# Kernel tuning notes

Hardware: AMD Instinct MI355X
Metric: run time of the kernel (lower is better)

Reference implementation:

```python
import jax, jax.numpy as jnp
import numpy as np


def setup_inputs() -> dict:
    key = jax.random.key(0)
    k1, k2 = jax.random.split(key)
    B, N, M = 8, 8192, 8192
    xyz1 = jax.random.normal(k1, (B, N, 3), dtype=jnp.float32)
    xyz2 = jax.random.normal(k2, (B, M, 3), dtype=jnp.float32)
    return {"xyz1": xyz1, "xyz2": xyz2}


def reference(xyz1, xyz2):
    # (same math as the CUDA kernel's per-pair squared L2 scan).
    sq1 = jnp.sum(xyz1 * xyz1, axis=-1)              # [B, N]
    sq2 = jnp.sum(xyz2 * xyz2, axis=-1)              # [B, M]
    inner = jnp.einsum('bnd,bmd->bnm', xyz1, xyz2)   # [B, N, M]
    d = sq1[:, :, None] + sq2[:, None, :] - 2.0 * inner
    d = jnp.maximum(d, 0.0)  # guard tiny negatives from the expansion
    dist1 = jnp.min(d, axis=2)  # [B, N] nearest sq-dist in xyz2 for each xyz1 point
    dist2 = jnp.min(d, axis=1)  # [B, M] nearest sq-dist in xyz1 for each xyz2 point
    return dist1, dist2
```

## Files before the change

### kernel.cpp

```cpp
#include <hip/hip_runtime.h>
#include <math.h>


typedef __attribute__((ext_vector_type(8))) short short8;
typedef __attribute__((ext_vector_type(16))) float f32x16;

#define CTC    256
#define TILEB  (CTC * 32)
#define NGRP   (CTC / 32)
#define NSPLIT 4

__host__ __device__ static inline size_t pad512(size_t x) {
  return (x + 511) & ~(size_t)511;
}

__device__ __forceinline__ unsigned short bf16h(float x) {
  unsigned u = __float_as_uint(x);
  return (unsigned short)((u + 0x7fffu + ((u >> 16) & 1u)) >> 16);
}
__device__ __forceinline__ float bf16f(unsigned short h) {
  return __uint_as_float((unsigned)h << 16);
}
__device__ __forceinline__ float m3(float a, float b, float c) {
  return fminf(fminf(a, b), c);
}
__device__ __forceinline__ float red16(const f32x16& d, float mm) {
  float r0 = m3(d[0], d[1], d[2]);
  float r1 = m3(d[3], d[4], d[5]);
  float r2 = m3(d[6], d[7], d[8]);
  float r3 = m3(d[9], d[10], d[11]);
  float r4 = m3(d[12], d[13], d[14]);
  return m3(m3(r0, r1, r2), m3(r3, r4, d[15]), mm);
}

#define GLOAD_LDS16(gp, sp)                                                   \
  __builtin_amdgcn_global_load_lds(                                           \
      (const __attribute__((address_space(1))) unsigned int*)(gp),            \
      (__attribute__((address_space(3))) unsigned int*)(sp), 16, 0, 0)

__global__ __launch_bounds__(256) void frag_kernel(
    const float* __restrict__ xyz1, const float* __restrict__ xyz2,
    char* __restrict__ frags, int B, int N, int M)
{
  const int z = blockIdx.z, dir = z / B, b = z % B;
  const size_t Mpad = pad512((size_t)M), Npad = pad512((size_t)N);
  const float* cp; char* reg_; int Nc; size_t Pc;
  if (dir == 0) {
    cp = xyz2 + (size_t)b * M * 3;
    reg_ = frags + (size_t)b * Mpad * 32;
    Nc = M; Pc = Mpad;
  } else {
    cp = xyz1 + (size_t)b * N * 3;
    reg_ = frags + (size_t)B * Mpad * 32 + (size_t)b * Npad * 32;
    Nc = N; Pc = Npad;
  }
  const size_t j = (size_t)blockIdx.x * 256 + threadIdx.x;
  if (j >= Pc) return;

  float x = 0.f, y = 0.f, zz = 0.f, sq = 3.0e38f;
  if (j < (size_t)Nc) {
    x = cp[3 * j + 0]; y = cp[3 * j + 1]; zz = cp[3 * j + 2];
    sq = x * x; sq = fmaf(y, y, sq); sq = fmaf(zz, zz, sq);
  }
  const float ex = -2.f * x, ey = -2.f * y, ez = -2.f * zz;
  const unsigned short ehx = bf16h(ex); const unsigned short elx = bf16h(ex - bf16f(ehx));
  const unsigned short ehy = bf16h(ey); const unsigned short ely = bf16h(ey - bf16f(ehy));
  const unsigned short ehz = bf16h(ez); const unsigned short elz = bf16h(ez - bf16f(ehz));
  const unsigned short sh  = bf16h(sq); const unsigned short sl  = bf16h(sq - bf16f(sh));

  short8 f0, f1;
  f0[0] = (short)ehx; f0[1] = (short)ehy; f0[2] = (short)ehz; f0[3] = (short)elx;
  f0[4] = (short)ely; f0[5] = (short)elz; f0[6] = (short)ehx; f0[7] = (short)ehy;
  f1[0] = (short)ehz; f1[1] = (short)elx; f1[2] = (short)ely; f1[3] = (short)elz;
  f1[4] = (short)sh;  f1[5] = (short)sl;  f1[6] = 0;          f1[7] = 0;

  short8* fp = (short8*)reg_ + ((j >> 5) * 64 + (j & 31));
  fp[0]  = f0;
  fp[32] = f1;
}

__device__ __forceinline__ short8 make_qfrag(float x, float y, float z, int hi) {
  const unsigned short hx = bf16h(x); const unsigned short lx = bf16h(x - bf16f(hx));
  const unsigned short hy = bf16h(y); const unsigned short ly = bf16h(y - bf16f(hy));
  const unsigned short hz = bf16h(z); const unsigned short lz = bf16h(z - bf16f(hz));
  const unsigned short ONE = 0x3F80;
  short8 f;
  if (hi == 0) {
    f[0] = (short)hx; f[1] = (short)hy; f[2] = (short)hz; f[3] = (short)hx;
    f[4] = (short)hy; f[5] = (short)hz; f[6] = (short)lx; f[7] = (short)ly;
  } else {
    f[0] = (short)lz; f[1] = (short)lx; f[2] = (short)ly; f[3] = (short)lz;
    f[4] = (short)ONE; f[5] = (short)ONE; f[6] = 0; f[7] = 0;
  }
  return f;
}

__global__ __launch_bounds__(256, 8) void chamfer_mfma(
    const float* __restrict__ xyz1, const float* __restrict__ xyz2,
    const char* __restrict__ frags, float* __restrict__ out,
    int B, int N, int M)
{
  const int z = blockIdx.z, dir = z / B, b = z % B;
  const size_t Mpad = pad512((size_t)M), Npad = pad512((size_t)N);
  const float* qp; float* o; const char* fr; int Nq, Nc;
  if (dir == 0) {
    qp = xyz1 + (size_t)b * N * 3;
    o  = out + (size_t)b * N;
    fr = frags + (size_t)b * Mpad * 32;
    Nq = N; Nc = (int)Mpad;
  } else {
    qp = xyz2 + (size_t)b * M * 3;
    o  = out + (size_t)B * N + (size_t)b * M;
    fr = frags + (size_t)B * Mpad * 32 + (size_t)b * Npad * 32;
    Nq = M; Nc = (int)Npad;
  }
  if ((int)(blockIdx.x * 256) >= Nq) return;

  const int ntT = Nc / CTC;
  const int hT  = (ntT + NSPLIT - 1) / NSPLIT;
  const int t0  = blockIdx.y * hT;
  const int t1  = (t0 + hT < ntT) ? (t0 + hT) : ntT;
  const int nt  = t1 - t0;
  if (nt <= 0) return;
  const char* frh = fr + (size_t)t0 * TILEB;

  const int lane = threadIdx.x & 63;
  const int wid  = threadIdx.x >> 6;
  const int hi   = lane >> 5;

  const int qbase = blockIdx.x * 256 + wid * 64;
  const int n0 = qbase + (lane & 31);
  const int n1 = n0 + 32;
  const int n0c = n0 < Nq ? n0 : Nq - 1;
  const int n1c = n1 < Nq ? n1 : Nq - 1;
  const float q0x = qp[3 * n0c], q0y = qp[3 * n0c + 1], q0z = qp[3 * n0c + 2];
  const float q1x = qp[3 * n1c], q1y = qp[3 * n1c + 1], q1z = qp[3 * n1c + 2];
  float sqq0 = q0x * q0x; sqq0 = fmaf(q0y, q0y, sqq0); sqq0 = fmaf(q0z, q0z, sqq0);
  float sqq1 = q1x * q1x; sqq1 = fmaf(q1y, q1y, sqq1); sqq1 = fmaf(q1z, q1z, sqq1);
  const short8 bq0 = make_qfrag(q0x, q0y, q0z, hi);
  const short8 bq1 = make_qfrag(q1x, q1y, q1z, hi);

  __shared__ __align__(16) char lds[2][TILEB];

  {
    const char* src = frh + wid * 1024 + lane * 16;
    char* dst = lds[0] + wid * 1024;
#pragma unroll
    for (int i = 0; i < 2; ++i)
      GLOAD_LDS16(src + i * 4096, dst + i * 4096);
  }

  f32x16 zacc = {0.f,0.f,0.f,0.f,0.f,0.f,0.f,0.f,0.f,0.f,0.f,0.f,0.f,0.f,0.f,0.f};
  float mm0 = 3.0e38f, mm1 = 3.0e38f;

  for (int t = 0; t < nt; ++t) {
    asm volatile("s_waitcnt vmcnt(0)" ::: "memory");
    __syncthreads();
    if (t + 1 < nt) {
      const char* src = frh + (size_t)(t + 1) * TILEB + wid * 1024 + lane * 16;
      char* dst = lds[(t + 1) & 1] + wid * 1024;
#pragma unroll
      for (int i = 0; i < 2; ++i)
        GLOAD_LDS16(src + i * 4096, dst + i * 4096);
    }
    const char* bc = lds[t & 1] + lane * 16;
#pragma unroll 4
    for (int g = 0; g < NGRP; ++g) {
      const short8 fa = *(const short8*)(bc + g * 1024);
      const f32x16 da = __builtin_amdgcn_mfma_f32_32x32x16_bf16(fa, bq0, zacc, 0, 0, 0);
      const f32x16 db = __builtin_amdgcn_mfma_f32_32x32x16_bf16(fa, bq1, zacc, 0, 0, 0);
      mm0 = red16(da, mm0);
      mm1 = red16(db, mm1);
    }
  }

  mm0 = fminf(mm0, __shfl_xor(mm0, 32));
  mm1 = fminf(mm1, __shfl_xor(mm1, 32));
  if (lane < 32) {
    if (n0 < Nq) atomicMin((unsigned int*)(o + n0), __float_as_uint(fmaxf(mm0 + sqq0, 0.f)));
    if (n1 < Nq) atomicMin((unsigned int*)(o + n1), __float_as_uint(fmaxf(mm1 + sqq1, 0.f)));
  }
}

extern "C" void kernel_launch(void* const* d_in, const int* in_sizes, int n_in,
                              void* d_out, int out_size, void* d_ws, size_t ws_size,
                              hipStream_t stream) {
  const float* xyz1 = (const float*)d_in[0];
  const float* xyz2 = (const float*)d_in[1];
  float* out = (float*)d_out;

  const int B = 8;
  const int N = in_sizes[0] / (B * 3);
  const int M = in_sizes[1] / (B * 3);

  hipMemsetAsync(d_out, 0x7f, (size_t)out_size * sizeof(float), stream);

  const size_t Npad = pad512((size_t)N), Mpad = pad512((size_t)M);
  char* frags = (char*)d_ws;

  const size_t pmax = Npad > Mpad ? Npad : Mpad;
  dim3 g1((unsigned)(pmax / 256), 1, 2 * B);
  frag_kernel<<<g1, dim3(256), 0, stream>>>(xyz1, xyz2, frags, B, N, M);

  const int nmax = N > M ? N : M;
  dim3 g2((unsigned)((nmax + 255) / 256), NSPLIT, 2 * B);
  chamfer_mfma<<<g2, dim3(256), 0, stream>>>(xyz1, xyz2, frags, out, B, N, M);
}
```

Before: 94.22 us.

## Stream candidate fragments directly from global memory with register prefetch instead of LDS

Drops the double-buffered LDS staging and its per-tile block barriers. Each wave now reads its short8 fragments straight from global memory, relying on L1/L2 reuse across the four waves, and prefetches the next fragments into registers one step ahead. MFMA issue is wrapped in s_setprio raises, and the 3D grid is flattened to 1D with the batch/direction index varying fastest, which changes block scheduling order and cache locality. The prefetch reads up to two fragment groups past each split's range, and the same waves now fetch duplicate data through the vector memory path.

Result: no change. 92.78 us (-1.5%).

```diff
diff --git a/kernel.cpp b/kernel.cpp
--- a/kernel.cpp
+++ b/kernel.cpp
@@ -5,9 +5,6 @@
 typedef __attribute__((ext_vector_type(8))) short short8;
 typedef __attribute__((ext_vector_type(16))) float f32x16;
 
-#define CTC    256
-#define TILEB  (CTC * 32)
-#define NGRP   (CTC / 32)
 #define NSPLIT 4
 
 __host__ __device__ static inline size_t pad512(size_t x) {
@@ -32,11 +29,6 @@
   float r4 = m3(d[12], d[13], d[14]);
   return m3(m3(r0, r1, r2), m3(r3, r4, d[15]), mm);
 }
-
-#define GLOAD_LDS16(gp, sp)                                                   \
-  __builtin_amdgcn_global_load_lds(                                           \
-      (const __attribute__((address_space(1))) unsigned int*)(gp),            \
-      (__attribute__((address_space(3))) unsigned int*)(sp), 16, 0, 0)
 
 __global__ __launch_bounds__(256) void frag_kernel(
     const float* __restrict__ xyz1, const float* __restrict__ xyz2,
@@ -100,7 +92,13 @@
     const char* __restrict__ frags, float* __restrict__ out,
     int B, int N, int M)
 {
-  const int z = blockIdx.z, dir = z / B, b = z % B;
+  const int id   = (int)blockIdx.x;
+  const int z    = id % (2 * B);
+  const int rest = id / (2 * B);
+  const int by   = rest % NSPLIT;
+  const int bx   = rest / NSPLIT;
+
+  const int dir = z / B, b = z % B;
   const size_t Mpad = pad512((size_t)M), Npad = pad512((size_t)N);
   const float* qp; float* o; const char* fr; int Nq, Nc;
   if (dir == 0) {
@@ -114,21 +112,16 @@
     fr = frags + (size_t)B * Mpad * 32 + (size_t)b * Npad * 32;
     Nq = M; Nc = (int)Npad;
   }
-  if ((int)(blockIdx.x * 256) >= Nq) return;
-
-  const int ntT = Nc / CTC;
-  const int hT  = (ntT + NSPLIT - 1) / NSPLIT;
-  const int t0  = blockIdx.y * hT;
-  const int t1  = (t0 + hT < ntT) ? (t0 + hT) : ntT;
-  const int nt  = t1 - t0;
-  if (nt <= 0) return;
-  const char* frh = fr + (size_t)t0 * TILEB;
+  if (bx * 256 >= Nq) return;
 
   const int lane = threadIdx.x & 63;
   const int wid  = threadIdx.x >> 6;
   const int hi   = lane >> 5;
 
-  const int qbase = blockIdx.x * 256 + wid * 64;
+  const int gq = Nc / (32 * NSPLIT);
+  const char* gp = fr + (size_t)by * gq * 1024 + (size_t)lane * 16;
+
+  const int qbase = bx * 256 + wid * 64;
   const int n0 = qbase + (lane & 31);
   const int n1 = n0 + 32;
   const int n0c = n0 < Nq ? n0 : Nq - 1;
@@ -140,38 +133,30 @@
   const short8 bq0 = make_qfrag(q0x, q0y, q0z, hi);
   const short8 bq1 = make_qfrag(q1x, q1y, q1z, hi);
 
-  __shared__ __align__(16) char lds[2][TILEB];
-
-  {
-    const char* src = frh + wid * 1024 + lane * 16;
-    char* dst = lds[0] + wid * 1024;
-#pragma unroll
-    for (int i = 0; i < 2; ++i)
-      GLOAD_LDS16(src + i * 4096, dst + i * 4096);
-  }
-
-  f32x16 zacc = {0.f,0.f,0.f,0.f,0.f,0.f,0.f,0.f,0.f,0.f,0.f,0.f,0.f,0.f,0.f,0.f};
+  const f32x16 zacc = {0.f,0.f,0.f,0.f,0.f,0.f,0.f,0.f,
+                       0.f,0.f,0.f,0.f,0.f,0.f,0.f,0.f};
   float mm0 = 3.0e38f, mm1 = 3.0e38f;
 
-  for (int t = 0; t < nt; ++t) {
-    asm volatile("s_waitcnt vmcnt(0)" ::: "memory");
-    __syncthreads();
-    if (t + 1 < nt) {
-      const char* src = frh + (size_t)(t + 1) * TILEB + wid * 1024 + lane * 16;
-      char* dst = lds[(t + 1) & 1] + wid * 1024;
-#pragma unroll
-      for (int i = 0; i < 2; ++i)
-        GLOAD_LDS16(src + i * 4096, dst + i * 4096);
-    }
-    const char* bc = lds[t & 1] + lane * 16;
-#pragma unroll 4
-    for (int g = 0; g < NGRP; ++g) {
-      const short8 fa = *(const short8*)(bc + g * 1024);
-      const f32x16 da = __builtin_amdgcn_mfma_f32_32x32x16_bf16(fa, bq0, zacc, 0, 0, 0);
-      const f32x16 db = __builtin_amdgcn_mfma_f32_32x32x16_bf16(fa, bq1, zacc, 0, 0, 0);
-      mm0 = red16(da, mm0);
-      mm1 = red16(db, mm1);
-    }
+  short8 f0 = *(const short8*)(gp);
+  short8 f1 = *(const short8*)(gp + 1024);
+  for (int g = 0; g < gq; g += 2) {
+    const short8 nf0 = *(const short8*)(gp + (size_t)(g + 2) * 1024);
+    __builtin_amdgcn_s_setprio(1);
+    const f32x16 da = __builtin_amdgcn_mfma_f32_32x32x16_bf16(f0, bq0, zacc, 0, 0, 0);
+    const f32x16 db = __builtin_amdgcn_mfma_f32_32x32x16_bf16(f0, bq1, zacc, 0, 0, 0);
+    __builtin_amdgcn_s_setprio(0);
+    mm0 = red16(da, mm0);
+    mm1 = red16(db, mm1);
+    f0 = nf0;
+
+    const short8 nf1 = *(const short8*)(gp + (size_t)(g + 3) * 1024);
+    __builtin_amdgcn_s_setprio(1);
+    const f32x16 dc = __builtin_amdgcn_mfma_f32_32x32x16_bf16(f1, bq0, zacc, 0, 0, 0);
+    const f32x16 dd = __builtin_amdgcn_mfma_f32_32x32x16_bf16(f1, bq1, zacc, 0, 0, 0);
+    __builtin_amdgcn_s_setprio(0);
+    mm0 = red16(dc, mm0);
+    mm1 = red16(dd, mm1);
+    f1 = nf1;
   }
 
   mm0 = fminf(mm0, __shfl_xor(mm0, 32));
@@ -203,6 +188,7 @@
   frag_kernel<<<g1, dim3(256), 0, stream>>>(xyz1, xyz2, frags, B, N, M);
 
   const int nmax = N > M ? N : M;
-  dim3 g2((unsigned)((nmax + 255) / 256), NSPLIT, 2 * B);
+  const unsigned nx = (unsigned)((nmax + 255) / 256);
+  dim3 g2(nx * NSPLIT * 2 * B, 1, 1);
   chamfer_mfma<<<g2, dim3(256), 0, stream>>>(xyz1, xyz2, frags, out, B, N, M);
 }
```
